# Performance work log

Measured on AMD Instinct MI355X. Metric: run time of the kernel, lower is better.

The kernel has to match this reference:

```python
import jax, jax.numpy as jnp
import numpy as np

EPS_SHIFT = 1e-8   # additive epsilon used by the original code
EPS_NORM = 1e-12   # torch.nn.functional.normalize default eps


def setup_inputs() -> dict:
    key = jax.random.key(0)
    inputs = jax.random.normal(key, (1024, 2048, 3, 3), dtype=jnp.float32)
    return {"inputs": inputs}


def reference(inputs):
    # inputs: (B, num_res, 3, 3) -> flat atom chain (B, N, 3), N = 3*num_res
    B, R = inputs.shape[0], inputs.shape[1]
    x = inputs.reshape(B, R * 3, 3)

    # sliding 4-atom windows, vectorized over all N-3 dihedrals
    a = x[:, :-3, :]
    b = x[:, 1:-2, :]
    c = x[:, 2:-1, :]
    d = x[:, 3:, :]

    bc_raw = b - c + EPS_SHIFT
    bc = bc_raw / jnp.clip(
        jnp.linalg.norm(bc_raw, axis=-1, keepdims=True), EPS_NORM)

    n1 = jnp.cross(a - b, bc)          # (B, N-3, 3)
    n2 = jnp.cross(bc, c - d)          # (B, N-3, 3)
    xc = jnp.sum(n1 * n2, axis=-1)     # (B, N-3)
    yc = jnp.sum(jnp.cross(n1, bc) * n2, axis=-1)
    dih = jnp.arctan2(yc, xc + EPS_SHIFT)

    # original concatenates all sin values then all cos values along last dim
    angles = jnp.concatenate([jnp.sin(dih), jnp.cos(dih)], axis=-1)  # (B, 2*(N-3))
    first_three = x[:, :3, :]                                        # (B, 3, 3)
    return (angles, first_three)
```

## Files before the change

kernel.cpp:

```cpp
#include <hip/hip_runtime.h>

#define ROWS 1024
#define PTS 6144
#define NDIH (PTS - 3)
#define ROWF (PTS * 3)
#define CHUNK 1024
#define DPT 4
#define THREADS 256
#define NCHUNK 6
#define ANG_PER_ROW (2 * NDIH)
#define SFLOATS ((CHUNK + 3) * 3 + 3)
#define EPS_SHIFT 1e-8f

__global__ __launch_bounds__(THREADS) void dih_kernel(const float* __restrict__ in,
                                                      float* __restrict__ out) {
    __shared__ float s[SFLOATS];
    const int b     = blockIdx.x / NCHUNK;
    const int chunk = blockIdx.x % NCHUNK;
    const int i0    = chunk * CHUNK;
    const int t     = threadIdx.x;

    const float* row = in + (size_t)b * ROWF;
    const int base = i0 * 3;
    const int n4 = min(SFLOATS / 4, (ROWF - base) / 4);
    const float4* g4 = (const float4*)(row + base);
    float4* s4 = (float4*)s;
    for (int k = t; k < n4; k += THREADS) s4[k] = g4[k];
    __syncthreads();

    if (chunk == 0 && t < 9)
        out[(size_t)ROWS * ANG_PER_ROW + (size_t)b * 9 + t] = s[t];

    float w[21];
    {
        const float4* ls4 = (const float4*)(s + 12 * t);
        float4 v0 = ls4[0], v1 = ls4[1], v2 = ls4[2], v3 = ls4[3], v4 = ls4[4];
        w[0]=v0.x;  w[1]=v0.y;  w[2]=v0.z;  w[3]=v0.w;
        w[4]=v1.x;  w[5]=v1.y;  w[6]=v1.z;  w[7]=v1.w;
        w[8]=v2.x;  w[9]=v2.y;  w[10]=v2.z; w[11]=v2.w;
        w[12]=v3.x; w[13]=v3.y; w[14]=v3.z; w[15]=v3.w;
        w[16]=v4.x; w[17]=v4.y; w[18]=v4.z; w[19]=v4.w;
        w[20]=s[12 * t + 20];
    }

    float ex[6], ey[6], ez[6];
    #pragma unroll
    for (int j = 0; j < 6; ++j) {
        ex[j] = w[3*j + 0] - w[3*j + 3];
        ey[j] = w[3*j + 1] - w[3*j + 4];
        ez[j] = w[3*j + 2] - w[3*j + 5];
    }

    float sv[DPT], cv[DPT];
    #pragma unroll
    for (int k = 0; k < DPT; ++k) {
        const float brx = ex[k+1] + EPS_SHIFT;
        const float bry = ey[k+1] + EPS_SHIFT;
        const float brz = ez[k+1] + EPS_SHIFT;
        const float nrm2 = brx*brx + bry*bry + brz*brz;
        const float inv = rsqrtf(fmaxf(nrm2, 1e-24f));
        const float ux = brx * inv, uy = bry * inv, uz = brz * inv;

        const float n1x = ey[k]*uz - ez[k]*uy;
        const float n1y = ez[k]*ux - ex[k]*uz;
        const float n1z = ex[k]*uy - ey[k]*ux;
        const float n2x = uy*ez[k+2] - uz*ey[k+2];
        const float n2y = uz*ex[k+2] - ux*ez[k+2];
        const float n2z = ux*ey[k+2] - uy*ex[k+2];

        const float xc = n1x*n2x + n1y*n2y + n1z*n2z;
        const float mx = n1y*uz - n1z*uy;
        const float my = n1z*ux - n1x*uz;
        const float mz = n1x*uy - n1y*ux;
        const float yc = mx*n2x + my*n2y + mz*n2z;

        const float xz = xc + EPS_SHIFT;
        const float r2 = yc*yc + xz*xz;
        const float rinv = rsqrtf(fmaxf(r2, 1e-30f));
        sv[k] = (r2 > 0.0f) ? yc * rinv : 0.0f;
        cv[k] = (r2 > 0.0f) ? xz * rinv : 1.0f;
    }

    __syncthreads();
    ((float4*)s)[t]           = make_float4(sv[0], sv[1], sv[2], sv[3]);
    ((float4*)(s + CHUNK))[t] = make_float4(cv[0], cv[1], cv[2], cv[3]);
    __syncthreads();

    const size_t obase = (size_t)b * ANG_PER_ROW;
    const int valid = min(CHUNK, NDIH - i0);
    float* so = out + obase + i0;
    float* co = out + obase + NDIH + i0;
    #pragma unroll
    for (int k = 0; k < 4; ++k) {
        const int j = k * THREADS + t;
        if (j < valid) {
            so[j] = s[j];
            co[j] = s[CHUNK + j];
        }
    }
}

extern "C" void kernel_launch(void* const* d_in, const int* in_sizes, int n_in,
                              void* d_out, int out_size, void* d_ws, size_t ws_size,
                              hipStream_t stream) {
    const float* in = (const float*)d_in[0];
    float* out = (float*)d_out;
    dih_kernel<<<dim3(ROWS * NCHUNK), dim3(THREADS), 0, stream>>>(in, out);
}
```

Measured before the change: 120.1 us.

## Drop shared-memory staging; load windows from global and use nontemporal stores

Removes the LDS staging buffer and both barriers. Each thread now reads its 24-float window straight from global memory as vector loads that overlap with neighbouring threads, relying on the cache for reuse. Outputs are written directly with nontemporal stores: sines as a float4, cosines as four scalar stores because the cos segment is misaligned at NDIH offset. The aim is to cut LDS traffic and synchronisation, at the cost of redundant global loads and less coalesced, unaligned cos stores.

After: 120.8 us. No clear change (+0.6%).

```diff
diff --git a/kernel.cpp b/kernel.cpp
--- a/kernel.cpp
+++ b/kernel.cpp
@@ -2,45 +2,45 @@
 
 #define ROWS 1024
 #define PTS 6144
-#define NDIH (PTS - 3)
-#define ROWF (PTS * 3)
-#define CHUNK 1024
-#define DPT 4
+#define NDIH 6141
+#define ROWF 18432
+#define TPR 1536
 #define THREADS 256
 #define NCHUNK 6
-#define ANG_PER_ROW (2 * NDIH)
-#define SFLOATS ((CHUNK + 3) * 3 + 3)
+#define ANG_PER_ROW 12282
 #define EPS_SHIFT 1e-8f
+
+typedef float vfloat4 __attribute__((ext_vector_type(4)));
 
 __global__ __launch_bounds__(THREADS) void dih_kernel(const float* __restrict__ in,
                                                       float* __restrict__ out) {
-    __shared__ float s[SFLOATS];
     const int b     = blockIdx.x / NCHUNK;
     const int chunk = blockIdx.x % NCHUNK;
-    const int i0    = chunk * CHUNK;
-    const int t     = threadIdx.x;
+    const int T     = chunk * THREADS + threadIdx.x;
+    const float* row = in + (size_t)b * ROWF;
 
-    const float* row = in + (size_t)b * ROWF;
-    const int base = i0 * 3;
-    const int n4 = min(SFLOATS / 4, (ROWF - base) / 4);
-    const float4* g4 = (const float4*)(row + base);
-    float4* s4 = (float4*)s;
-    for (int k = t; k < n4; k += THREADS) s4[k] = g4[k];
-    __syncthreads();
+    if (chunk == 0 && threadIdx.x < 9) {
+        __builtin_nontemporal_store(row[threadIdx.x],
+            out + (size_t)ROWS * ANG_PER_ROW + (size_t)b * 9 + threadIdx.x);
+    }
 
-    if (chunk == 0 && t < 9)
-        out[(size_t)ROWS * ANG_PER_ROW + (size_t)b * 9 + t] = s[t];
-
-    float w[21];
+    const bool full = (T < TPR - 1);
+    const vfloat4* g4 = (const vfloat4*)(row + 12 * T);
+    float w[24];
     {
-        const float4* ls4 = (const float4*)(s + 12 * t);
-        float4 v0 = ls4[0], v1 = ls4[1], v2 = ls4[2], v3 = ls4[3], v4 = ls4[4];
+        const vfloat4 v0 = g4[0], v1 = g4[1], v2 = g4[2];
         w[0]=v0.x;  w[1]=v0.y;  w[2]=v0.z;  w[3]=v0.w;
         w[4]=v1.x;  w[5]=v1.y;  w[6]=v1.z;  w[7]=v1.w;
         w[8]=v2.x;  w[9]=v2.y;  w[10]=v2.z; w[11]=v2.w;
-        w[12]=v3.x; w[13]=v3.y; w[14]=v3.z; w[15]=v3.w;
-        w[16]=v4.x; w[17]=v4.y; w[18]=v4.z; w[19]=v4.w;
-        w[20]=s[12 * t + 20];
+        if (full) {
+            const vfloat4 v3 = g4[3], v4 = g4[4], v5 = g4[5];
+            w[12]=v3.x; w[13]=v3.y; w[14]=v3.z; w[15]=v3.w;
+            w[16]=v4.x; w[17]=v4.y; w[18]=v4.z; w[19]=v4.w;
+            w[20]=v5.x; w[21]=v5.y; w[22]=v5.z; w[23]=v5.w;
+        } else {
+            #pragma unroll
+            for (int k = 12; k < 24; ++k) w[k] = 0.0f;
+        }
     }
 
     float ex[6], ey[6], ez[6];
@@ -51,9 +51,9 @@
         ez[j] = w[3*j + 2] - w[3*j + 5];
     }
 
-    float sv[DPT], cv[DPT];
+    float sv[4], cv[4];
     #pragma unroll
-    for (int k = 0; k < DPT; ++k) {
+    for (int k = 0; k < 4; ++k) {
         const float brx = ex[k+1] + EPS_SHIFT;
         const float bry = ey[k+1] + EPS_SHIFT;
         const float brz = ez[k+1] + EPS_SHIFT;
@@ -81,22 +81,20 @@
         cv[k] = (r2 > 0.0f) ? xz * rinv : 1.0f;
     }
 
-    __syncthreads();
-    ((float4*)s)[t]           = make_float4(sv[0], sv[1], sv[2], sv[3]);
-    ((float4*)(s + CHUNK))[t] = make_float4(cv[0], cv[1], cv[2], cv[3]);
-    __syncthreads();
-
+    const int i = 4 * T;
     const size_t obase = (size_t)b * ANG_PER_ROW;
-    const int valid = min(CHUNK, NDIH - i0);
-    float* so = out + obase + i0;
-    float* co = out + obase + NDIH + i0;
-    #pragma unroll
-    for (int k = 0; k < 4; ++k) {
-        const int j = k * THREADS + t;
-        if (j < valid) {
-            so[j] = s[j];
-            co[j] = s[CHUNK + j];
-        }
+    if (full) {
+        vfloat4 sv4;
+        sv4.x = sv[0]; sv4.y = sv[1]; sv4.z = sv[2]; sv4.w = sv[3];
+        __builtin_nontemporal_store(sv4, (vfloat4*)(out + obase + i));
+        float* co = out + obase + NDIH + i;
+        __builtin_nontemporal_store(cv[0], co + 0);
+        __builtin_nontemporal_store(cv[1], co + 1);
+        __builtin_nontemporal_store(cv[2], co + 2);
+        __builtin_nontemporal_store(cv[3], co + 3);
+    } else {
+        __builtin_nontemporal_store(sv[0], out + obase + i);
+        __builtin_nontemporal_store(cv[0], out + obase + NDIH + i);
     }
 }
 
```
